# Kernel tuning notes

Measured on AMD Instinct MI355X. Metric: run time of the kernel, lower is better.

## Reference

```python
import jax, jax.numpy as jnp
import numpy as np
from jax import lax

EPS = 1e-06
NUM_FEATURES = 2048


def _welford(xr, mean0, var0):
    """Sequential Welford running mean/var, exactly matching the torch loop.

    xr: [N, F] rows processed one at a time.
    Update for the n-th observation (n starts at 1):
      if n > 1: var = (n-2)/(n-1)*var + (obs-mean)^2/n
      mean += (obs-mean)/n
    """
    n_rows = xr.shape[0]

    def step(carry, inp):
        mean, var = carry
        obs, n = inp
        nf = n.astype(xr.dtype)
        d = obs - mean
        # safe denominator so the unselected branch at n==1 is finite
        var_new = jnp.where(n > 1, (nf - 2.0) / jnp.maximum(nf - 1.0, 1.0) * var + d * d / nf, var)
        mean_new = mean + d / nf
        return (mean_new, var_new), None

    ns = jnp.arange(1, n_rows + 1, dtype=jnp.int32)
    (mean, var), _ = lax.scan(step, (mean0, var0), (xr, ns))
    return mean, var


def setup_inputs() -> dict:
    key = jax.random.key(0)
    x = jax.random.normal(key, (8192, NUM_FEATURES), dtype=jnp.float32)
    running_mean = jnp.zeros((NUM_FEATURES,), dtype=jnp.float32)
    running_var = jnp.ones((NUM_FEATURES,), dtype=jnp.float32)
    return {"x": x, "running_mean": running_mean, "running_var": running_var}


def reference(x, running_mean, running_var):
    xr = x.reshape(-1, NUM_FEATURES)
    mean, var = _welford(xr, running_mean, running_var)
    # normalize with the FINAL running stats (loop completes before return)
    return (x - mean) / jnp.sqrt(var + EPS)
```

## Files before the change

### kernel.cpp

```cpp
#include <hip/hip_runtime.h>

constexpr int F = 2048;
constexpr int NROWS = 8192;
constexpr float EPS = 1e-6f;
constexpr int STRIDE4 = F / 4;

__global__ __launch_bounds__(256) void reduce_kernel(const float* __restrict__ x,
                                                     float* __restrict__ acc) {
    __shared__ float4 lS[3 * 64];
    __shared__ float4 lQ[3 * 64];

    const int lc = threadIdx.x & 63;
    const int sg = threadIdx.x >> 6;
    const int c4 = blockIdx.x * 64 + lc;
    const int row0 = blockIdx.y * 64 + sg * 16;
    const float4* __restrict__ xv = reinterpret_cast<const float4*>(x);

    float4 s = make_float4(0.f, 0.f, 0.f, 0.f);
    float4 q = make_float4(0.f, 0.f, 0.f, 0.f);

    size_t base = (size_t)row0 * STRIDE4 + (size_t)c4;
#pragma unroll
    for (int r = 0; r < 16; ++r) {
        float4 v = xv[base + (size_t)r * STRIDE4];
        s.x += v.x;  s.y += v.y;  s.z += v.z;  s.w += v.w;
        q.x += v.x * v.x;  q.y += v.y * v.y;  q.z += v.z * v.z;  q.w += v.w * v.w;
    }

    if (sg != 0) {
        lS[(sg - 1) * 64 + lc] = s;
        lQ[(sg - 1) * 64 + lc] = q;
    }
    __syncthreads();

    if (sg == 0) {
#pragma unroll
        for (int k = 0; k < 3; ++k) {
            float4 t = lS[k * 64 + lc];
            float4 u = lQ[k * 64 + lc];
            s.x += t.x;  s.y += t.y;  s.z += t.z;  s.w += t.w;
            q.x += u.x;  q.y += u.y;  q.z += u.z;  q.w += u.w;
        }
        float* __restrict__ sum   = acc;
        float* __restrict__ sumsq = acc + F;
        const int c = c4 * 4;
        atomicAdd(&sum[c + 0], s.x);
        atomicAdd(&sum[c + 1], s.y);
        atomicAdd(&sum[c + 2], s.z);
        atomicAdd(&sum[c + 3], s.w);
        atomicAdd(&sumsq[c + 0], q.x);
        atomicAdd(&sumsq[c + 1], q.y);
        atomicAdd(&sumsq[c + 2], q.z);
        atomicAdd(&sumsq[c + 3], q.w);
    }
}

__global__ void finalize_kernel(const float* __restrict__ acc, float* __restrict__ stats) {
    const int c = blockIdx.x * blockDim.x + threadIdx.x;
    if (c < F) {
        const float s1 = acc[c];
        const float s2 = acc[c + F];
        const float invN = 1.0f / (float)NROWS;
        const float mean = s1 * invN;
        float var = (s2 - s1 * mean) * (1.0f / (float)(NROWS - 1));
        var = fmaxf(var, 0.0f);
        const float r = rsqrtf(var + EPS);
        stats[c]     = r;
        stats[c + F] = -mean * r;
    }
}

constexpr int TOTAL4 = NROWS * STRIDE4;
constexpr int HALF4  = TOTAL4 / 2;

__global__ __launch_bounds__(256) void normalize_kernel(const float* __restrict__ x,
                                                        const float* __restrict__ stats,
                                                        float* __restrict__ out) {
    const size_t i = (size_t)blockIdx.x * blockDim.x + threadIdx.x;
    const float4* __restrict__ xv = reinterpret_cast<const float4*>(x);
    float4* __restrict__ ov       = reinterpret_cast<float4*>(out);
    const float4* __restrict__ rv = reinterpret_cast<const float4*>(stats);
    const float4* __restrict__ bv = reinterpret_cast<const float4*>(stats + F);

#pragma unroll
    for (int h = 0; h < 2; ++h) {
        const size_t idx = i + (size_t)h * HALF4;
        const int c4 = (int)(idx & (STRIDE4 - 1));
        float4 v = xv[idx];
        float4 r = rv[c4];
        float4 b = bv[c4];
        float4 o;
        o.x = fmaf(v.x, r.x, b.x);
        o.y = fmaf(v.y, r.y, b.y);
        o.z = fmaf(v.z, r.z, b.z);
        o.w = fmaf(v.w, r.w, b.w);
        ov[idx] = o;
    }
}

extern "C" void kernel_launch(void* const* d_in, const int* in_sizes, int n_in,
                              void* d_out, int out_size, void* d_ws, size_t ws_size,
                              hipStream_t stream) {
    const float* x = (const float*)d_in[0];
    float* out   = (float*)d_out;
    float* acc   = (float*)d_ws;
    float* stats = acc + 2 * F;

    hipMemsetAsync(d_ws, 0, 2 * F * sizeof(float), stream);

    reduce_kernel<<<dim3(8, NROWS / 64), 256, 0, stream>>>(x, acc);
    finalize_kernel<<<F / 256, 256, 0, stream>>>(acc, stats);
    normalize_kernel<<<HALF4 / 256, 256, 0, stream>>>(x, stats, out);
}
```

Measured before the change: 132.8 us.

## Fuse reduce, finalize and normalize into one persistent kernel with grid barrier

Replaces the three launches with a single kernel of 512 blocks. Each thread keeps its 32 rows of x in registers, the column sums go through atomics, and a global spin barrier waits until all blocks have contributed before the stats are computed locally. The output is then written from the registers, so x is read from HBM once instead of twice and two launches go away. The cost is very high register pressure (128 VGPRs for the data alone), and correctness depends on all 512 blocks being co-resident; the barrier has a guard counter that breaks out on timeout.

Result: slower. 172.0 us (+29.5%).

```diff
diff --git a/kernel.cpp b/kernel.cpp
--- a/kernel.cpp
+++ b/kernel.cpp
@@ -3,28 +3,45 @@
 constexpr int F = 2048;
 constexpr int NROWS = 8192;
 constexpr float EPS = 1e-6f;
-constexpr int STRIDE4 = F / 4;
+constexpr int S4 = F / 4;
 
-__global__ __launch_bounds__(256) void reduce_kernel(const float* __restrict__ x,
-                                                     float* __restrict__ acc) {
+constexpr int NBLOCKS = 512;
+constexpr int RPT = 32;
+
+
+__global__ __launch_bounds__(256, 2) void fused_kernel(const float* __restrict__ x,
+                                                       float* __restrict__ out,
+                                                       float* __restrict__ acc,
+                                                       unsigned* __restrict__ bar) {
     __shared__ float4 lS[3 * 64];
     __shared__ float4 lQ[3 * 64];
+    __shared__ float  sr[256];
+    __shared__ float  sb[256];
 
-    const int lc = threadIdx.x & 63;
-    const int sg = threadIdx.x >> 6;
-    const int c4 = blockIdx.x * 64 + lc;
-    const int row0 = blockIdx.y * 64 + sg * 16;
+    const int tid = threadIdx.x;
+    const int lc  = tid & 63;
+    const int sg  = tid >> 6;
+    const int cg  = blockIdx.x & 7;
+    const int rg  = blockIdx.x >> 3;
+    const int c4  = cg * 64 + lc;
+    const int row0 = rg * 128 + sg * 32;
+
     const float4* __restrict__ xv = reinterpret_cast<const float4*>(x);
+    float4* __restrict__ ov       = reinterpret_cast<float4*>(out);
 
+    float4 v[RPT];
     float4 s = make_float4(0.f, 0.f, 0.f, 0.f);
     float4 q = make_float4(0.f, 0.f, 0.f, 0.f);
-
-    size_t base = (size_t)row0 * STRIDE4 + (size_t)c4;
+    const size_t base = (size_t)row0 * S4 + (size_t)c4;
 #pragma unroll
-    for (int r = 0; r < 16; ++r) {
-        float4 v = xv[base + (size_t)r * STRIDE4];
-        s.x += v.x;  s.y += v.y;  s.z += v.z;  s.w += v.w;
-        q.x += v.x * v.x;  q.y += v.y * v.y;  q.z += v.z * v.z;  q.w += v.w * v.w;
+    for (int r = 0; r < RPT; ++r) {
+        v[r] = xv[base + (size_t)r * S4];
+    }
+#pragma unroll
+    for (int r = 0; r < RPT; ++r) {
+        s.x += v[r].x;  s.y += v[r].y;  s.z += v[r].z;  s.w += v[r].w;
+        q.x += v[r].x * v[r].x;  q.y += v[r].y * v[r].y;
+        q.z += v[r].z * v[r].z;  q.w += v[r].w * v[r].w;
     }
 
     if (sg != 0) {
@@ -32,7 +49,6 @@
         lQ[(sg - 1) * 64 + lc] = q;
     }
     __syncthreads();
-
     if (sg == 0) {
 #pragma unroll
         for (int k = 0; k < 3; ++k) {
@@ -53,48 +69,43 @@
         atomicAdd(&sumsq[c + 2], q.z);
         atomicAdd(&sumsq[c + 3], q.w);
     }
-}
 
-__global__ void finalize_kernel(const float* __restrict__ acc, float* __restrict__ stats) {
-    const int c = blockIdx.x * blockDim.x + threadIdx.x;
-    if (c < F) {
-        const float s1 = acc[c];
-        const float s2 = acc[c + F];
-        const float invN = 1.0f / (float)NROWS;
-        const float mean = s1 * invN;
+    __syncthreads();
+    if (tid == 0) {
+        __threadfence();
+        atomicAdd(bar, 1u);
+        int guard = 0;
+        while (atomicAdd(bar, 0u) < (unsigned)NBLOCKS) {
+            __builtin_amdgcn_s_sleep(2);
+            if (++guard > (1 << 27)) break;
+        }
+        __threadfence();
+    }
+    __syncthreads();
+
+    {
+        const int col = cg * 256 + tid;
+        const float s1 = acc[col];
+        const float s2 = acc[col + F];
+        const float mean = s1 * (1.0f / (float)NROWS);
         float var = (s2 - s1 * mean) * (1.0f / (float)(NROWS - 1));
         var = fmaxf(var, 0.0f);
         const float r = rsqrtf(var + EPS);
-        stats[c]     = r;
-        stats[c + F] = -mean * r;
+        sr[tid] = r;
+        sb[tid] = -mean * r;
     }
-}
+    __syncthreads();
 
-constexpr int TOTAL4 = NROWS * STRIDE4;
-constexpr int HALF4  = TOTAL4 / 2;
-
-__global__ __launch_bounds__(256) void normalize_kernel(const float* __restrict__ x,
-                                                        const float* __restrict__ stats,
-                                                        float* __restrict__ out) {
-    const size_t i = (size_t)blockIdx.x * blockDim.x + threadIdx.x;
-    const float4* __restrict__ xv = reinterpret_cast<const float4*>(x);
-    float4* __restrict__ ov       = reinterpret_cast<float4*>(out);
-    const float4* __restrict__ rv = reinterpret_cast<const float4*>(stats);
-    const float4* __restrict__ bv = reinterpret_cast<const float4*>(stats + F);
-
+    const float4 r4 = reinterpret_cast<const float4*>(sr)[lc];
+    const float4 b4 = reinterpret_cast<const float4*>(sb)[lc];
 #pragma unroll
-    for (int h = 0; h < 2; ++h) {
-        const size_t idx = i + (size_t)h * HALF4;
-        const int c4 = (int)(idx & (STRIDE4 - 1));
-        float4 v = xv[idx];
-        float4 r = rv[c4];
-        float4 b = bv[c4];
+    for (int r = 0; r < RPT; ++r) {
         float4 o;
-        o.x = fmaf(v.x, r.x, b.x);
-        o.y = fmaf(v.y, r.y, b.y);
-        o.z = fmaf(v.z, r.z, b.z);
-        o.w = fmaf(v.w, r.w, b.w);
-        ov[idx] = o;
+        o.x = fmaf(v[r].x, r4.x, b4.x);
+        o.y = fmaf(v[r].y, r4.y, b4.y);
+        o.z = fmaf(v[r].z, r4.z, b4.z);
+        o.w = fmaf(v[r].w, r4.w, b4.w);
+        ov[base + (size_t)r * S4] = o;
     }
 }
 
@@ -102,13 +113,11 @@
                               void* d_out, int out_size, void* d_ws, size_t ws_size,
                               hipStream_t stream) {
     const float* x = (const float*)d_in[0];
-    float* out   = (float*)d_out;
-    float* acc   = (float*)d_ws;
-    float* stats = acc + 2 * F;
+    float* out    = (float*)d_out;
+    float* acc    = (float*)d_ws;
+    unsigned* bar = (unsigned*)((char*)d_ws + 2 * F * sizeof(float));
 
-    hipMemsetAsync(d_ws, 0, 2 * F * sizeof(float), stream);
+    hipMemsetAsync(d_ws, 0, 2 * F * sizeof(float) + 64, stream);
 
-    reduce_kernel<<<dim3(8, NROWS / 64), 256, 0, stream>>>(x, acc);
-    finalize_kernel<<<F / 256, 256, 0, stream>>>(acc, stats);
-    normalize_kernel<<<HALF4 / 256, 256, 0, stream>>>(x, stats, out);
+    fused_kernel<<<NBLOCKS, 256, 0, stream>>>(x, out, acc, bar);
 }
```
